# Kernel tuning notes

Measured on AMD Instinct MI355X. Metric: run time of the kernel, lower is better.

The kernel has to match this reference:

```python
import jax, jax.numpy as jnp
import numpy as np

F = 16      # frames
NV = 4096   # visual points per frame
NT = 512    # tactile points per frame
M = 4096    # model points
SCALE = 0.1


def setup_inputs() -> dict:
    key = jax.random.key(0)
    ks = jax.random.split(key, 6)
    return {
        "state": jax.random.normal(ks[0], (6,), dtype=jnp.float32) * 0.1,
        "model_points": jax.random.normal(ks[1], (M, 3), dtype=jnp.float32),
        "visual_points": jax.random.normal(ks[2], (F, NV, 3), dtype=jnp.float32),
        "tactile_points": jax.random.normal(ks[3], (F, NT, 3), dtype=jnp.float32),
        "physics_pred_states": jax.random.normal(ks[4], (F, 12), dtype=jnp.float32) * 0.1,
        "delta_time": jax.random.uniform(ks[5], (F,), dtype=jnp.float32, minval=0.01, maxval=0.05),
    }


def _skew(a):
    z = jnp.zeros((), a.dtype)
    return jnp.array([[z, -a[2], a[1]],
                      [a[2], z, -a[0]],
                      [-a[1], a[0], z]])


def _rot_from_omega(omega, dt):
    # Rodrigues: R = I + sin(theta*dt) S + (1 - cos(theta*dt)) S@S, S = skew(omega/|omega|)
    theta = jnp.linalg.norm(omega)
    ax = omega / jnp.clip(theta, 1e-8)
    S = _skew(ax)
    return jnp.eye(3, dtype=omega.dtype) + jnp.sin(theta * dt) * S + (1.0 - jnp.cos(theta * dt)) * (S @ S)


def _chamfer(pred, gt):
    # rows: pred [N,3], cols: gt [M,3]; row-min of squared distances, then mean
    d = (jnp.sum(pred * pred, axis=1)[:, None]
         + jnp.sum(gt * gt, axis=1)[None, :]
         - 2.0 * pred @ gt.T)
    return jnp.mean(jnp.min(d, axis=1))


def reference(state, model_points, visual_points, tactile_points, physics_pred_states, delta_time):
    t0 = state[:3]
    r0 = _rot_from_omega(state[3:], jnp.float32(1.0))  # Euler2Mat modeled as axis-angle

    def pose_step(carry, x):
        t, r = carry
        v, omega, dt = x
        t = t + v * dt
        r = _rot_from_omega(omega, dt) @ r
        return (t, r), (t, r)

    _, (ts, rs) = jax.lax.scan(
        pose_step, (t0, r0),
        (physics_pred_states[1:, 6:9], physics_pred_states[1:, 9:12], delta_time[1:]))
    ts = jnp.concatenate([t0[None], ts], axis=0)  # [F,3]
    rs = jnp.concatenate([r0[None], rs], axis=0)  # [F,3,3]

    def frame_loss(acc, x):
        t, r, vp, tp = x
        vc = ((vp - t) @ r) / SCALE
        tc = ((tp - t) @ r) / SCALE
        acc = acc + _chamfer(vc, model_points) + 0.1 * _chamfer(tc, model_points)
        return acc, None

    E_cd, _ = jax.lax.scan(frame_loss, jnp.zeros((), jnp.float32),
                           (ts, rs, visual_points, tactile_points))
    return E_cd
```

## Files before the change

kernel.cpp:

```cpp
#include <hip/hip_runtime.h>
#include <math.h>

#define F_    16
#define NV_   4096
#define NT_   512
#define M_    4096
#define PPF_  (NV_ + NT_)
#define NPTS_ (F_ * PPF_)
#define SCALE_INV 10.0f

#define TPB   256
#define PTSB  72
#define NBLK  (NPTS_ / PTSB)
#define NG    32
#define MPG   (M_ / NG)
#define CHM   32
#define NCH   (MPG / CHM)
#define FS    33
#define PPL   9

__device__ inline void rot_from_omega(float ox, float oy, float oz, float dt,
                                      float* R) {
    float theta = sqrtf(ox * ox + oy * oy + oz * oz);
    float inv = 1.0f / fmaxf(theta, 1e-8f);
    float ax = ox * inv, ay = oy * inv, az = oz * inv;
    float s = sinf(theta * dt);
    float c = 1.0f - cosf(theta * dt);
    R[0] = 1.0f - c * (ay * ay + az * az);
    R[1] = -s * az + c * ax * ay;
    R[2] =  s * ay + c * ax * az;
    R[3] =  s * az + c * ax * ay;
    R[4] = 1.0f - c * (ax * ax + az * az);
    R[5] = -s * ax + c * ay * az;
    R[6] = -s * ay + c * ax * az;
    R[7] =  s * ax + c * ay * az;
    R[8] = 1.0f - c * (ax * ax + ay * ay);
}

__global__ __launch_bounds__(TPB, 4) void chamfer_one(
    const float* __restrict__ state, const float* __restrict__ model,
    const float* __restrict__ vis, const float* __restrict__ tac,
    const float* __restrict__ phys, const float* __restrict__ dts,
    float* __restrict__ out) {
    __shared__ float4 feat[NG * FS];
    __shared__ float  sdm[PTSB][NG + 1];
    __shared__ float  sw[2];

    const int t  = threadIdx.x;
    const int g  = t >> 3;
    const int m0 = t & 7;
    const int pl = t & 7;
    const int f  = (blockIdx.x * PTSB) / PPF_;
    const int lbase = blockIdx.x * PTSB - f * PPF_;

#pragma unroll
    for (int j2 = 0; j2 < 4; ++j2) {
        int id = g * MPG + m0 + 8 * j2;
        float gx = model[id * 3 + 0], gy = model[id * 3 + 1], gz = model[id * 3 + 2];
        feat[g * FS + m0 + 8 * j2] =
            make_float4(-2.0f * gx, -2.0f * gy, -2.0f * gz, gx * gx + gy * gy + gz * gz);
    }

    float R[9], tr[3];
    {
        tr[0] = state[0]; tr[1] = state[1]; tr[2] = state[2];
        rot_from_omega(state[3], state[4], state[5], 1.0f, R);
        for (int i = 1; i <= f; ++i) {
            float dt = dts[i];
            tr[0] += phys[i * 12 + 6] * dt;
            tr[1] += phys[i * 12 + 7] * dt;
            tr[2] += phys[i * 12 + 8] * dt;
            float Rs[9];
            rot_from_omega(phys[i * 12 + 9], phys[i * 12 + 10], phys[i * 12 + 11], dt, Rs);
            float Rn[9];
            for (int r = 0; r < 3; ++r)
                for (int c2 = 0; c2 < 3; ++c2)
                    Rn[r * 3 + c2] = Rs[r * 3 + 0] * R[0 + c2] +
                                     Rs[r * 3 + 1] * R[3 + c2] +
                                     Rs[r * 3 + 2] * R[6 + c2];
            for (int j = 0; j < 9; ++j) R[j] = Rn[j];
        }
        for (int j = 0; j < 9; ++j) R[j] *= SCALE_INV;
    }

    float c0[PPL], c1[PPL], c2[PPL], cn[PPL], dm[PPL];
#pragma unroll
    for (int k = 0; k < PPL; ++k) {
        int loc = lbase + pl * PPL + k;
        const float* p = (loc < NV_) ? (vis + ((size_t)f * NV_ + loc) * 3)
                                     : (tac + ((size_t)f * NT_ + (loc - NV_)) * 3);
        float d0 = p[0] - tr[0], d1 = p[1] - tr[1], d2 = p[2] - tr[2];
        float x = d0 * R[0] + d1 * R[3] + d2 * R[6];
        float y = d0 * R[1] + d1 * R[4] + d2 * R[7];
        float z = d0 * R[2] + d1 * R[5] + d2 * R[8];
        c0[k] = x; c1[k] = y; c2[k] = z;
        cn[k] = x * x + y * y + z * z;
        dm[k] = 3.4e38f;
    }
    __syncthreads();

    for (int c = 0; c < NCH; ++c) {
        float mx[4], my[4], mz[4];
        if (c + 1 < NCH) {
#pragma unroll
            for (int j2 = 0; j2 < 4; ++j2) {
                int id = g * MPG + (c + 1) * CHM + m0 + 8 * j2;
                mx[j2] = model[id * 3 + 0];
                my[j2] = model[id * 3 + 1];
                mz[j2] = model[id * 3 + 2];
            }
        }
        const float4* fb = &feat[g * FS];
#pragma unroll 4
        for (int m = 0; m < CHM; m += 2) {
            float4 ga = fb[m];
            float4 gb = fb[m + 1];
#pragma unroll
            for (int k = 0; k < PPL; ++k) {
                float da = fmaf(ga.x, c0[k], fmaf(ga.y, c1[k], fmaf(ga.z, c2[k], ga.w)));
                float db = fmaf(gb.x, c0[k], fmaf(gb.y, c1[k], fmaf(gb.z, c2[k], gb.w)));
                dm[k] = fminf(fminf(da, db), dm[k]);
            }
        }
        __syncthreads();
        if (c + 1 < NCH) {
#pragma unroll
            for (int j2 = 0; j2 < 4; ++j2) {
                feat[g * FS + m0 + 8 * j2] =
                    make_float4(-2.0f * mx[j2], -2.0f * my[j2], -2.0f * mz[j2],
                                mx[j2] * mx[j2] + my[j2] * my[j2] + mz[j2] * mz[j2]);
            }
            __syncthreads();
        }
    }

#pragma unroll
    for (int k = 0; k < PPL; ++k) sdm[pl * PPL + k][g] = dm[k] + cn[k];
    __syncthreads();

    float v = 0.0f;
    if (t < PTSB) {
        const float* row = sdm[t];
        float mn = row[0];
#pragma unroll
        for (int i = 1; i < NG; ++i) mn = fminf(mn, row[i]);
        const int loc = lbase + t;
        const float w = (loc < NV_) ? (1.0f / NV_) : (0.1f / NT_);
        v = mn * w;
    }
    if (t < 128) {
#pragma unroll
        for (int off = 32; off > 0; off >>= 1) v += __shfl_down(v, off);
        if ((t & 63) == 0) sw[t >> 6] = v;
    }
    __syncthreads();
    if (t == 0) atomicAdd(out, sw[0] + sw[1]);
}

extern "C" void kernel_launch(void* const* d_in, const int* in_sizes, int n_in,
                              void* d_out, int out_size, void* d_ws, size_t ws_size,
                              hipStream_t stream) {
    const float* state = (const float*)d_in[0];
    const float* model = (const float*)d_in[1];
    const float* vis   = (const float*)d_in[2];
    const float* tac   = (const float*)d_in[3];
    const float* phys  = (const float*)d_in[4];
    const float* dts   = (const float*)d_in[5];
    float* out = (float*)d_out;
    (void)d_ws; (void)ws_size;

    hipMemsetAsync(out, 0, sizeof(float), stream);
    chamfer_one<<<NBLK, TPB, 0, stream>>>(state, model, vis, tac, phys, dts, out);
}
```

Measured before the change: 105.7 us.

## Use packed FP32 FMA inline asm for distance loop and raise points per lane

Replaces the scalar FMA distance computation with hand-written v_pk_fma_f32 inline assembly that evaluates two points per instruction. Points per lane go from 9 to 12 and points per block from 72 to 96, so the block count drops. Occupancy hint is lowered to 3 blocks per CU to allow more registers. The aim is to roughly halve FMA issue count in the hot loop; it risks register pressure, less scheduling freedom around the inline asm, and fewer blocks to spread across CUs.

```diff
diff --git a/kernel.cpp b/kernel.cpp
--- a/kernel.cpp
+++ b/kernel.cpp
@@ -10,14 +10,18 @@
 #define SCALE_INV 10.0f
 
 #define TPB   256
-#define PTSB  72
+#define PTSB  96
 #define NBLK  (NPTS_ / PTSB)
 #define NG    32
 #define MPG   (M_ / NG)
 #define CHM   32
 #define NCH   (MPG / CHM)
 #define FS    33
-#define PPL   9
+#define PPL   12
+#define NPR   6
+
+typedef float v2f __attribute__((ext_vector_type(2)));
+typedef float v4f __attribute__((ext_vector_type(4)));
 
 __device__ inline void rot_from_omega(float ox, float oy, float oz, float dt,
                                       float* R) {
@@ -37,14 +41,50 @@
     R[8] = 1.0f - c * (ax * ax + ay * ay);
 }
 
-__global__ __launch_bounds__(TPB, 4) void chamfer_one(
+__device__ __forceinline__ void dist6(v2f qa01, v2f qa23, v2f qb01, v2f qb23,
+                                      v2f c0a, v2f c0b, v2f c0c,
+                                      v2f c1a, v2f c1b, v2f c1c,
+                                      v2f c2a, v2f c2b, v2f c2c, float* dmp) {
+    v2f A0, A1, A2, B0, B1, B2;
+    asm("v_pk_fma_f32 %0, %7, %16, %7 op_sel:[0,0,1] op_sel_hi:[0,1,1]\n\t"
+        "v_pk_fma_f32 %1, %7, %17, %7 op_sel:[0,0,1] op_sel_hi:[0,1,1]\n\t"
+        "v_pk_fma_f32 %2, %7, %18, %7 op_sel:[0,0,1] op_sel_hi:[0,1,1]\n\t"
+        "v_pk_fma_f32 %3, %9, %16, %9 op_sel:[0,0,1] op_sel_hi:[0,1,1]\n\t"
+        "v_pk_fma_f32 %4, %9, %17, %9 op_sel:[0,0,1] op_sel_hi:[0,1,1]\n\t"
+        "v_pk_fma_f32 %5, %9, %18, %9 op_sel:[0,0,1] op_sel_hi:[0,1,1]\n\t"
+        "v_pk_fma_f32 %0, %6, %13, %0 op_sel:[1,0,0] op_sel_hi:[1,1,1]\n\t"
+        "v_pk_fma_f32 %1, %6, %14, %1 op_sel:[1,0,0] op_sel_hi:[1,1,1]\n\t"
+        "v_pk_fma_f32 %2, %6, %15, %2 op_sel:[1,0,0] op_sel_hi:[1,1,1]\n\t"
+        "v_pk_fma_f32 %3, %8, %13, %3 op_sel:[1,0,0] op_sel_hi:[1,1,1]\n\t"
+        "v_pk_fma_f32 %4, %8, %14, %4 op_sel:[1,0,0] op_sel_hi:[1,1,1]\n\t"
+        "v_pk_fma_f32 %5, %8, %15, %5 op_sel:[1,0,0] op_sel_hi:[1,1,1]\n\t"
+        "v_pk_fma_f32 %0, %6, %10, %0 op_sel:[0,0,0] op_sel_hi:[0,1,1]\n\t"
+        "v_pk_fma_f32 %1, %6, %11, %1 op_sel:[0,0,0] op_sel_hi:[0,1,1]\n\t"
+        "v_pk_fma_f32 %2, %6, %12, %2 op_sel:[0,0,0] op_sel_hi:[0,1,1]\n\t"
+        "v_pk_fma_f32 %3, %8, %10, %3 op_sel:[0,0,0] op_sel_hi:[0,1,1]\n\t"
+        "v_pk_fma_f32 %4, %8, %11, %4 op_sel:[0,0,0] op_sel_hi:[0,1,1]\n\t"
+        "v_pk_fma_f32 %5, %8, %12, %5 op_sel:[0,0,0] op_sel_hi:[0,1,1]"
+        : "=&v"(A0), "=&v"(A1), "=&v"(A2), "=&v"(B0), "=&v"(B1), "=&v"(B2)
+        : "v"(qa01), "v"(qa23), "v"(qb01), "v"(qb23),
+          "v"(c0a), "v"(c0b), "v"(c0c),
+          "v"(c1a), "v"(c1b), "v"(c1c),
+          "v"(c2a), "v"(c2b), "v"(c2c));
+    dmp[0] = fminf(fminf(A0.x, B0.x), dmp[0]);
+    dmp[1] = fminf(fminf(A0.y, B0.y), dmp[1]);
+    dmp[2] = fminf(fminf(A1.x, B1.x), dmp[2]);
+    dmp[3] = fminf(fminf(A1.y, B1.y), dmp[3]);
+    dmp[4] = fminf(fminf(A2.x, B2.x), dmp[4]);
+    dmp[5] = fminf(fminf(A2.y, B2.y), dmp[5]);
+}
+
+__global__ __launch_bounds__(TPB, 3) void chamfer_one(
     const float* __restrict__ state, const float* __restrict__ model,
     const float* __restrict__ vis, const float* __restrict__ tac,
     const float* __restrict__ phys, const float* __restrict__ dts,
     float* __restrict__ out) {
-    __shared__ float4 feat[NG * FS];
-    __shared__ float  sdm[PTSB][NG + 1];
-    __shared__ float  sw[2];
+    __shared__ v4f   feat[NG * FS];
+    __shared__ float sdm[PTSB][NG + 1];
+    __shared__ float sw[2];
 
     const int t  = threadIdx.x;
     const int g  = t >> 3;
@@ -58,7 +98,7 @@
         int id = g * MPG + m0 + 8 * j2;
         float gx = model[id * 3 + 0], gy = model[id * 3 + 1], gz = model[id * 3 + 2];
         feat[g * FS + m0 + 8 * j2] =
-            make_float4(-2.0f * gx, -2.0f * gy, -2.0f * gz, gx * gx + gy * gy + gz * gz);
+            (v4f){-2.0f * gx, -2.0f * gy, -2.0f * gz, gx * gx + gy * gy + gz * gz};
     }
 
     float R[9], tr[3];
@@ -83,7 +123,8 @@
         for (int j = 0; j < 9; ++j) R[j] *= SCALE_INV;
     }
 
-    float c0[PPL], c1[PPL], c2[PPL], cn[PPL], dm[PPL];
+    v2f c0p[NPR], c1p[NPR], c2p[NPR];
+    float cn[PPL], dm[PPL];
 #pragma unroll
     for (int k = 0; k < PPL; ++k) {
         int loc = lbase + pl * PPL + k;
@@ -93,9 +134,10 @@
         float x = d0 * R[0] + d1 * R[3] + d2 * R[6];
         float y = d0 * R[1] + d1 * R[4] + d2 * R[7];
         float z = d0 * R[2] + d1 * R[5] + d2 * R[8];
-        c0[k] = x; c1[k] = y; c2[k] = z;
         cn[k] = x * x + y * y + z * z;
         dm[k] = 3.4e38f;
+        if (k & 1) { c0p[k >> 1].y = x; c1p[k >> 1].y = y; c2p[k >> 1].y = z; }
+        else       { c0p[k >> 1].x = x; c1p[k >> 1].x = y; c2p[k >> 1].x = z; }
     }
     __syncthreads();
 
@@ -110,25 +152,25 @@
                 mz[j2] = model[id * 3 + 2];
             }
         }
-        const float4* fb = &feat[g * FS];
+        const v4f* fb = &feat[g * FS];
 #pragma unroll 4
         for (int m = 0; m < CHM; m += 2) {
-            float4 ga = fb[m];
-            float4 gb = fb[m + 1];
-#pragma unroll
-            for (int k = 0; k < PPL; ++k) {
-                float da = fmaf(ga.x, c0[k], fmaf(ga.y, c1[k], fmaf(ga.z, c2[k], ga.w)));
-                float db = fmaf(gb.x, c0[k], fmaf(gb.y, c1[k], fmaf(gb.z, c2[k], gb.w)));
-                dm[k] = fminf(fminf(da, db), dm[k]);
-            }
+            v4f ga = fb[m];
+            v4f gb = fb[m + 1];
+            v2f qa01 = (v2f){ga.x, ga.y}, qa23 = (v2f){ga.z, ga.w};
+            v2f qb01 = (v2f){gb.x, gb.y}, qb23 = (v2f){gb.z, gb.w};
+            dist6(qa01, qa23, qb01, qb23, c0p[0], c0p[1], c0p[2],
+                  c1p[0], c1p[1], c1p[2], c2p[0], c2p[1], c2p[2], dm);
+            dist6(qa01, qa23, qb01, qb23, c0p[3], c0p[4], c0p[5],
+                  c1p[3], c1p[4], c1p[5], c2p[3], c2p[4], c2p[5], dm + 6);
         }
         __syncthreads();
         if (c + 1 < NCH) {
 #pragma unroll
             for (int j2 = 0; j2 < 4; ++j2) {
                 feat[g * FS + m0 + 8 * j2] =
-                    make_float4(-2.0f * mx[j2], -2.0f * my[j2], -2.0f * mz[j2],
-                                mx[j2] * mx[j2] + my[j2] * my[j2] + mz[j2] * mz[j2]);
+                    (v4f){-2.0f * mx[j2], -2.0f * my[j2], -2.0f * mz[j2],
+                          mx[j2] * mx[j2] + my[j2] * my[j2] + mz[j2] * mz[j2]};
             }
             __syncthreads();
         }
```

After: 96.42 us. 8.8% less time.
